# Kernel tuning notes

Measured on AMD Instinct MI355X. Metric: run time of the kernel, lower is better.

Reference implementation:

```python
import jax, jax.numpy as jnp
import numpy as np

D_MODEL = 1024
NUM_HEADS = 16
DEPTH = D_MODEL // NUM_HEADS
B, S = 2, 2048


def setup_inputs() -> dict:
    key = jax.random.key(0)
    ks = jax.random.split(key, 12)
    s = 1.0 / np.sqrt(D_MODEL)
    return {
        "query": jax.random.normal(ks[0], (B, S, D_MODEL), jnp.float32),
        "key": jax.random.normal(ks[1], (B, S, D_MODEL), jnp.float32),
        "value": jax.random.normal(ks[2], (B, S, D_MODEL), jnp.float32),
        "mask": jax.random.randint(ks[3], (B, S), 0, 2, jnp.int32),
        "Wq": jax.random.normal(ks[4], (D_MODEL, D_MODEL), jnp.float32) * s,
        "bq": jnp.zeros((D_MODEL,), jnp.float32),
        "Wk": jax.random.normal(ks[5], (D_MODEL, D_MODEL), jnp.float32) * s,
        "bk": jnp.zeros((D_MODEL,), jnp.float32),
        "Wv": jax.random.normal(ks[6], (D_MODEL, D_MODEL), jnp.float32) * s,
        "bv": jnp.zeros((D_MODEL,), jnp.float32),
        "Wo": jax.random.normal(ks[7], (D_MODEL, D_MODEL), jnp.float32) * s,
        "bo": jnp.zeros((D_MODEL,), jnp.float32),
    }


def _split_heads(x):
    # [B, S, D] -> [B, H, S, depth]
    b, s, _ = x.shape
    return x.reshape(b, s, NUM_HEADS, DEPTH).transpose(0, 2, 1, 3)


def reference(query, key, value, mask, Wq, bq, Wk, bk, Wv, bv, Wo, bo):
    q = _split_heads(query @ Wq.T + bq)
    k = _split_heads(key @ Wk.T + bk)
    v = _split_heads(value @ Wv.T + bv)
    scale = 1.0 / jnp.sqrt(jnp.float32(DEPTH))
    # [B, H, Sq, Sk]
    logits = jnp.einsum("bhqd,bhkd->bhqk", q, k) * scale
    logits = logits + mask.astype(logits.dtype)[:, None, None, :] * (-1e9)
    attn = jax.nn.softmax(logits, axis=-1)
    out = jnp.einsum("bhqk,bhkd->bhqd", attn, v)
    out = out.transpose(0, 2, 1, 3).reshape(query.shape[0], -1, D_MODEL)
    return out @ Wo.T + bo
```

## Files before the change

### kernel.cpp

```cpp
#include <hip/hip_runtime.h>

typedef _Float16 half8 __attribute__((ext_vector_type(8)));
typedef float floatx4 __attribute__((ext_vector_type(4)));

#define D_MODEL 1024
#define NHEAD   16
#define DH      64
#define BATCH   2
#define SEQ     2048
#define M_TOT   4096

#define GLD_LDS16(g, l)                                                          \
  __builtin_amdgcn_global_load_lds(                                              \
      (const __attribute__((address_space(1))) void*)(g),                        \
      (__attribute__((address_space(3))) void*)(l), 16, 0, 0)

__global__ __launch_bounds__(256) void cvt_all(const float* __restrict__ q,
                                               const float* __restrict__ k,
                                               const float* __restrict__ v,
                                               const float* __restrict__ wq,
                                               const float* __restrict__ wk,
                                               const float* __restrict__ wv,
                                               const float* __restrict__ wo,
                                               _Float16* __restrict__ Xall,
                                               _Float16* __restrict__ Wall) {
  int bid = blockIdx.x;
  const float* src;
  _Float16* dst;
  if (bid < 6144) {
    int tsr = bid >> 11;
    src = (tsr == 0) ? q : (tsr == 1) ? k : v;
    dst = Xall + (size_t)tsr * 4194304;
    bid &= 2047;
  } else {
    int w = (bid - 6144) >> 9;
    src = (w == 0) ? wq : (w == 1) ? wk : (w == 2) ? wv : wo;
    dst = Wall + (size_t)w * 1048576;
    bid = (bid - 6144) & 511;
  }
  int off = bid * 2048 + threadIdx.x * 8;
  float4 a = *(const float4*)(src + off);
  float4 b = *(const float4*)(src + off + 4);
  half8 h;
  h[0] = (_Float16)a.x; h[1] = (_Float16)a.y; h[2] = (_Float16)a.z; h[3] = (_Float16)a.w;
  h[4] = (_Float16)b.x; h[5] = (_Float16)b.y; h[6] = (_Float16)b.z; h[7] = (_Float16)b.w;
  *(half8*)(dst + off) = h;
}

__global__ __launch_bounds__(256) void gemm_qkv(const _Float16* __restrict__ Xall,
                                                const _Float16* __restrict__ Wall,
                                                const float* __restrict__ bq,
                                                const float* __restrict__ bk,
                                                const float* __restrict__ bv,
                                                _Float16* __restrict__ Obase) {
  __shared__ alignas(16) char smem[17408];
  _Float16 (*As)[32]  = (_Float16(*)[32])smem;
  _Float16 (*Bs)[32]  = (_Float16(*)[32])(smem + 8192);
  _Float16 (*Ts)[136] = (_Float16(*)[136])smem;

  const int z = blockIdx.z;
  const _Float16* X = Xall + (size_t)z * 4194304;
  const _Float16* W = Wall + (size_t)z * 1048576;
  const float* bias = (z == 0) ? bq : (z == 1) ? bk : bv;
  _Float16* out = Obase + (size_t)z * 4194304;

  const int t = threadIdx.x, lane = t & 63, wave = t >> 6;
  const int wr = wave >> 1, wc = wave & 1;
  const int m0 = blockIdx.y * 128, n0 = blockIdx.x * 128;
  const int fr = lane & 15, fc = (lane >> 4) * 8, rg = (lane >> 4) * 4;

  floatx4 acc[4][4];
  for (int i = 0; i < 4; i++)
    for (int j = 0; j < 4; j++) acc[i][j] = (floatx4){0.f, 0.f, 0.f, 0.f};

  const int srow = lane >> 2, scol = (lane & 3) * 8;
  const _Float16* gA0 = X + (size_t)(m0 + wave * 32 + srow) * 1024 + scol;
  const _Float16* gA1 = gA0 + 16 * 1024;
  const _Float16* gB0 = W + (size_t)(n0 + wave * 32 + srow) * 1024 + scol;
  const _Float16* gB1 = gB0 + 16 * 1024;
  _Float16* lA0 = &As[wave * 32][0];
  _Float16* lA1 = &As[wave * 32 + 16][0];
  _Float16* lB0 = &Bs[wave * 32][0];
  _Float16* lB1 = &Bs[wave * 32 + 16][0];

  for (int k0 = 0; k0 < 1024; k0 += 32) {
    GLD_LDS16(gA0 + k0, lA0);
    GLD_LDS16(gA1 + k0, lA1);
    GLD_LDS16(gB0 + k0, lB0);
    GLD_LDS16(gB1 + k0, lB1);
    __syncthreads();

    half8 af[4], bw[4];
    for (int i = 0; i < 4; i++) {
      af[i] = *(const half8*)&As[wr * 64 + i * 16 + fr][fc];
      bw[i] = *(const half8*)&Bs[wc * 64 + i * 16 + fr][fc];
    }
    for (int i = 0; i < 4; i++)
      for (int j = 0; j < 4; j++)
        acc[i][j] = __builtin_amdgcn_mfma_f32_16x16x32_f16(af[i], bw[j], acc[i][j], 0, 0, 0);
    __syncthreads();
  }

  if (z != 2) {
    for (int i = 0; i < 4; i++)
      for (int j = 0; j < 4; j++) {
        int n = n0 + wc * 64 + j * 16 + fr;
        float bv2 = bias[n];
        int hh = n >> 6, d = n & 63;
        for (int r = 0; r < 4; r++) {
          int m = m0 + wr * 64 + i * 16 + rg + r;
          int bb = m >> 11, s = m & 2047;
          out[(((size_t)(bb * NHEAD + hh)) * SEQ + s) * DH + d] =
              (_Float16)(acc[i][j][r] + bv2);
        }
      }
  } else {
    const int bb = m0 >> 11, s0 = m0 & 2047;
    for (int p = 0; p < 2; p++) {
      __syncthreads();
      if (wc == p) {
        for (int j = 0; j < 4; j++) {
          float bv2 = bias[n0 + p * 64 + j * 16 + fr];
          for (int i = 0; i < 4; i++)
            for (int r = 0; r < 4; r++)
              Ts[j * 16 + fr][wr * 64 + i * 16 + rg + r] =
                  (_Float16)(acc[i][j][r] + bv2);
        }
      }
      __syncthreads();
      int dd = t >> 2, c4 = (t & 3) * 32;
      int hh = (n0 >> 6) + p;
      _Float16* dst = out + (((size_t)(bb * NHEAD + hh)) * DH + dd) * SEQ + s0;
      for (int u = 0; u < 4; u++)
        *(half8*)(dst + c4 + u * 8) = *(const half8*)&Ts[dd][c4 + u * 8];
    }
  }
}

__global__ __launch_bounds__(256) void gemm_wo(const _Float16* __restrict__ ctx,
                                               const _Float16* __restrict__ W,
                                               const float* __restrict__ bias,
                                               float* __restrict__ out) {
  __shared__ alignas(16) _Float16 As[128][32];
  __shared__ alignas(16) _Float16 Bs[64][32];

  const int t = threadIdx.x, lane = t & 63, wave = t >> 6;
  const int m0 = blockIdx.y * 128, n0 = blockIdx.x * 64;
  const int fr = lane & 15, fc = (lane >> 4) * 8, rg = (lane >> 4) * 4;

  floatx4 acc[2][4];
  for (int i = 0; i < 2; i++)
    for (int j = 0; j < 4; j++) acc[i][j] = (floatx4){0.f, 0.f, 0.f, 0.f};

  const int srow = lane >> 2, scol = (lane & 3) * 8;
  const _Float16* gA0 = ctx + (size_t)(m0 + wave * 32 + srow) * 1024 + scol;
  const _Float16* gA1 = gA0 + 16 * 1024;
  const _Float16* gB0 = W + (size_t)(n0 + wave * 16 + srow) * 1024 + scol;
  _Float16* lA0 = &As[wave * 32][0];
  _Float16* lA1 = &As[wave * 32 + 16][0];
  _Float16* lB0 = &Bs[wave * 16][0];

  for (int k0 = 0; k0 < 1024; k0 += 32) {
    GLD_LDS16(gA0 + k0, lA0);
    GLD_LDS16(gA1 + k0, lA1);
    GLD_LDS16(gB0 + k0, lB0);
    __syncthreads();

    half8 af[2], bw[4];
    for (int i = 0; i < 2; i++)
      af[i] = *(const half8*)&As[wave * 32 + i * 16 + fr][fc];
    for (int j = 0; j < 4; j++)
      bw[j] = *(const half8*)&Bs[j * 16 + fr][fc];
    for (int i = 0; i < 2; i++)
      for (int j = 0; j < 4; j++)
        acc[i][j] = __builtin_amdgcn_mfma_f32_16x16x32_f16(af[i], bw[j], acc[i][j], 0, 0, 0);
    __syncthreads();
  }

  for (int i = 0; i < 2; i++)
    for (int j = 0; j < 4; j++) {
      int n = n0 + j * 16 + fr;
      float bv2 = bias[n];
      for (int r = 0; r < 4; r++) {
        int m = m0 + wave * 32 + i * 16 + rg + r;
        out[(size_t)m * D_MODEL + n] = acc[i][j][r] + bv2;
      }
    }
}

__global__ __launch_bounds__(256) void attn_kernel(const _Float16* __restrict__ Qp,
                                                   const _Float16* __restrict__ Kp,
                                                   const _Float16* __restrict__ VT,
                                                   const int* __restrict__ mask,
                                                   _Float16* __restrict__ ctx) {
  __shared__ alignas(16) char lds[17408 + 34816 + 512];
  _Float16 (*Vt)[136] = (_Float16(*)[136])lds;
  _Float16 (*Ks)[72]  = (_Float16(*)[72])(lds + 17408);
  _Float16 (*Ps)[136] = (_Float16(*)[136])(lds + 17408);
  float* Ms = (float*)(lds + 17408 + 34816);

  const int b = blockIdx.z, h = blockIdx.y, q0 = blockIdx.x * 128;
  const int t = threadIdx.x, lane = t & 63, wave = t >> 6;
  const int fr = lane & 15, fc = (lane >> 4) * 8, rg = (lane >> 4) * 4;

  const _Float16* Kg  = Kp + (size_t)(b * NHEAD + h) * SEQ * DH;
  const _Float16* VTg = VT + (size_t)(b * NHEAD + h) * DH * SEQ;

  half8 qf[2][2];
  {
    const _Float16* Qgw = Qp + ((size_t)(b * NHEAD + h) * SEQ + q0 + wave * 32) * DH;
    for (int mi = 0; mi < 2; mi++)
      for (int kk = 0; kk < 2; kk++)
        qf[mi][kk] = *(const half8*)(Qgw + (mi * 16 + fr) * DH + kk * 32 + fc);
  }

  float mrow[2][4], lrow[2][4];
  floatx4 oacc[2][4];
  for (int mi = 0; mi < 2; mi++)
    for (int r = 0; r < 4; r++) { mrow[mi][r] = -3.0e38f; lrow[mi][r] = 0.f; }
  for (int mi = 0; mi < 2; mi++)
    for (int dj = 0; dj < 4; dj++) oacc[mi][dj] = (floatx4){0.f, 0.f, 0.f, 0.f};

  for (int kt = 0; kt < SEQ / 128; kt++) {
    const int k0 = kt * 128;
    {
      int r = t >> 1, c0 = (t & 1) * 32;
      const half8* gk = (const half8*)(Kg + (k0 + r) * 64 + c0);
      for (int u = 0; u < 4; u++)
        *(half8*)&Ks[r][c0 + u * 8] = gk[u];
      int dd = t >> 2, c4 = (t & 3) * 32;
      const _Float16* gv = VTg + (size_t)dd * SEQ + k0 + c4;
      for (int u = 0; u < 4; u++)
        *(half8*)&Vt[dd][c4 + u * 8] = *(const half8*)(gv + u * 8);
      if (t < 128) Ms[t] = (float)mask[b * SEQ + k0 + t] * -1.0e9f;
    }
    __syncthreads();

    floatx4 sa[2][8];
    for (int mi = 0; mi < 2; mi++)
      for (int nj = 0; nj < 8; nj++) sa[mi][nj] = (floatx4){0.f, 0.f, 0.f, 0.f};
    for (int nj = 0; nj < 8; nj++)
      for (int kk = 0; kk < 2; kk++) {
        half8 kf = *(const half8*)&Ks[nj * 16 + fr][kk * 32 + fc];
        sa[0][nj] = __builtin_amdgcn_mfma_f32_16x16x32_f16(qf[0][kk], kf, sa[0][nj], 0, 0, 0);
        sa[1][nj] = __builtin_amdgcn_mfma_f32_16x16x32_f16(qf[1][kk], kf, sa[1][nj], 0, 0, 0);
      }
    __syncthreads();

    for (int nj = 0; nj < 8; nj++) {
      float mk = Ms[nj * 16 + fr];
      for (int mi = 0; mi < 2; mi++)
        for (int r = 0; r < 4; r++)
          sa[mi][nj][r] = sa[mi][nj][r] * 0.125f + mk;
    }

    for (int mi = 0; mi < 2; mi++) {
      for (int r = 0; r < 4; r++) {
        float tm = sa[mi][0][r];
        for (int nj = 1; nj < 8; nj++) tm = fmaxf(tm, sa[mi][nj][r]);
        for (int off = 1; off < 16; off <<= 1) tm = fmaxf(tm, __shfl_xor(tm, off));
        float mnew = fmaxf(mrow[mi][r], tm);
        float alpha = __expf(mrow[mi][r] - mnew);
        mrow[mi][r] = mnew;
        float rs = 0.f;
        for (int nj = 0; nj < 8; nj++) {
          float p = __expf(sa[mi][nj][r] - mnew);
          sa[mi][nj][r] = p;
          rs += p;
        }
        for (int off = 1; off < 16; off <<= 1) rs += __shfl_xor(rs, off);
        lrow[mi][r] = lrow[mi][r] * alpha + rs;
        for (int dj = 0; dj < 4; dj++) oacc[mi][dj][r] *= alpha;
      }
    }

    for (int mi = 0; mi < 2; mi++)
      for (int nj = 0; nj < 8; nj++)
        for (int r = 0; r < 4; r++)
          Ps[wave * 32 + mi * 16 + rg + r][nj * 16 + fr] = (_Float16)sa[mi][nj][r];
    __syncthreads();

    for (int kk = 0; kk < 4; kk++) {
      half8 pf[2], vf[4];
      for (int mi = 0; mi < 2; mi++)
        pf[mi] = *(const half8*)&Ps[wave * 32 + mi * 16 + fr][kk * 32 + fc];
      for (int dj = 0; dj < 4; dj++)
        vf[dj] = *(const half8*)&Vt[dj * 16 + fr][kk * 32 + fc];
      for (int mi = 0; mi < 2; mi++)
        for (int dj = 0; dj < 4; dj++)
          oacc[mi][dj] = __builtin_amdgcn_mfma_f32_16x16x32_f16(pf[mi], vf[dj], oacc[mi][dj], 0, 0, 0);
    }
    __syncthreads();
  }

  for (int mi = 0; mi < 2; mi++)
    for (int r = 0; r < 4; r++) {
      float inv = 1.0f / lrow[mi][r];
      int qrow = q0 + wave * 32 + mi * 16 + rg + r;
      _Float16* o = ctx + ((size_t)b * SEQ + qrow) * D_MODEL + h * DH;
      for (int dj = 0; dj < 4; dj++)
        o[dj * 16 + fr] = (_Float16)(oacc[mi][dj][r] * inv);
    }
}

extern "C" void kernel_launch(void* const* d_in, const int* in_sizes, int n_in,
                              void* d_out, int out_size, void* d_ws, size_t ws_size,
                              hipStream_t stream) {
  const float* query = (const float*)d_in[0];
  const float* key   = (const float*)d_in[1];
  const float* value = (const float*)d_in[2];
  const int*   mask  = (const int*)d_in[3];
  const float* Wq = (const float*)d_in[4];
  const float* bq = (const float*)d_in[5];
  const float* Wk = (const float*)d_in[6];
  const float* bk = (const float*)d_in[7];
  const float* Wv = (const float*)d_in[8];
  const float* bv = (const float*)d_in[9];
  const float* Wo = (const float*)d_in[10];
  const float* bo = (const float*)d_in[11];

  char* ws = (char*)d_ws;
  _Float16* Xall = (_Float16*)(ws);
  _Float16* Wall = (_Float16*)(ws + (size_t)24 * 1024 * 1024);
  _Float16* Qp   = (_Float16*)(ws + (size_t)32 * 1024 * 1024);
  _Float16* ctx  = (_Float16*)(ws + (size_t)56 * 1024 * 1024);

  _Float16* Kp = Qp + (size_t)4194304;
  _Float16* VT = Qp + (size_t)8388608;

  cvt_all<<<8192, 256, 0, stream>>>(query, key, value, Wq, Wk, Wv, Wo, Xall, Wall);

  gemm_qkv<<<dim3(8, 32, 3), 256, 0, stream>>>(Xall, Wall, bq, bk, bv, Qp);

  attn_kernel<<<dim3(SEQ / 128, NHEAD, BATCH), 256, 0, stream>>>(Qp, Kp, VT, mask, ctx);

  gemm_wo<<<dim3(16, 32), 256, 0, stream>>>(ctx, Wall + (size_t)3 * 1048576, bo, (float*)d_out);
}
```

Before: 285.3 us.

## Compute transposed scores so P stays in registers, skipping LDS round-trip

The attention kernel now computes S^T = K·Q^T with MFMA, so each lane holds a column of scores for one query row. That lets the softmax P feed the PV MFMA (16x16x16) directly from registers, with no Ps write to LDS and two fewer barriers per key tile. Softmax uses exp2 with the scale and mask folded into a log2(e) factor, and row reductions need only two cross-lane shuffles. In exchange, the PV MFMA uses the smaller 16x16x16 shape, and P is converted to fp16 with round-toward-zero packing.

```diff
diff --git a/kernel.cpp b/kernel.cpp
--- a/kernel.cpp
+++ b/kernel.cpp
@@ -1,6 +1,8 @@
 #include <hip/hip_runtime.h>
 
 typedef _Float16 half8 __attribute__((ext_vector_type(8)));
+typedef _Float16 half4 __attribute__((ext_vector_type(4)));
+typedef __fp16  fp16x2 __attribute__((ext_vector_type(2)));
 typedef float floatx4 __attribute__((ext_vector_type(4)));
 
 #define D_MODEL 1024
@@ -10,10 +12,20 @@
 #define SEQ     2048
 #define M_TOT   4096
 
+#define SCALE_L2E 0.18033688011112042f
+#define MASK_L2E  (-1.4426950408889634e9f)
+
 #define GLD_LDS16(g, l)                                                          \
   __builtin_amdgcn_global_load_lds(                                              \
       (const __attribute__((address_space(1))) void*)(g),                        \
       (__attribute__((address_space(3))) void*)(l), 16, 0, 0)
+
+__device__ inline half4 pk4(floatx4 v) {
+  union { fp16x2 h2[2]; half4 h4; } u;
+  u.h2[0] = __builtin_amdgcn_cvt_pkrtz(v[0], v[1]);
+  u.h2[1] = __builtin_amdgcn_cvt_pkrtz(v[2], v[3]);
+  return u.h4;
+}
 
 __global__ __launch_bounds__(256) void cvt_all(const float* __restrict__ q,
                                                const float* __restrict__ k,
@@ -193,15 +205,13 @@
                                                    const _Float16* __restrict__ VT,
                                                    const int* __restrict__ mask,
                                                    _Float16* __restrict__ ctx) {
-  __shared__ alignas(16) char lds[17408 + 34816 + 512];
-  _Float16 (*Vt)[136] = (_Float16(*)[136])lds;
-  _Float16 (*Ks)[72]  = (_Float16(*)[72])(lds + 17408);
-  _Float16 (*Ps)[136] = (_Float16(*)[136])(lds + 17408);
-  float* Ms = (float*)(lds + 17408 + 34816);
+  __shared__ alignas(16) _Float16 Ks[128][72];
+  __shared__ alignas(16) _Float16 Vt[64][136];
+  __shared__ float Msf[128];
 
   const int b = blockIdx.z, h = blockIdx.y, q0 = blockIdx.x * 128;
   const int t = threadIdx.x, lane = t & 63, wave = t >> 6;
-  const int fr = lane & 15, fc = (lane >> 4) * 8, rg = (lane >> 4) * 4;
+  const int fr = lane & 15, quad = lane >> 4, fc = quad * 8;
 
   const _Float16* Kg  = Kp + (size_t)(b * NHEAD + h) * SEQ * DH;
   const _Float16* VTg = VT + (size_t)(b * NHEAD + h) * DH * SEQ;
@@ -214,12 +224,10 @@
         qf[mi][kk] = *(const half8*)(Qgw + (mi * 16 + fr) * DH + kk * 32 + fc);
   }
 
-  float mrow[2][4], lrow[2][4];
-  floatx4 oacc[2][4];
-  for (int mi = 0; mi < 2; mi++)
-    for (int r = 0; r < 4; r++) { mrow[mi][r] = -3.0e38f; lrow[mi][r] = 0.f; }
-  for (int mi = 0; mi < 2; mi++)
-    for (int dj = 0; dj < 4; dj++) oacc[mi][dj] = (floatx4){0.f, 0.f, 0.f, 0.f};
+  float mrow[2] = {-3.0e38f, -3.0e38f}, lrow[2] = {0.f, 0.f};
+  floatx4 oaccT[4][2];
+  for (int dj = 0; dj < 4; dj++)
+    for (int mi = 0; mi < 2; mi++) oaccT[dj][mi] = (floatx4){0.f, 0.f, 0.f, 0.f};
 
   for (int kt = 0; kt < SEQ / 128; kt++) {
     const int k0 = kt * 128;
@@ -232,75 +240,86 @@
       const _Float16* gv = VTg + (size_t)dd * SEQ + k0 + c4;
       for (int u = 0; u < 4; u++)
         *(half8*)&Vt[dd][c4 + u * 8] = *(const half8*)(gv + u * 8);
-      if (t < 128) Ms[t] = (float)mask[b * SEQ + k0 + t] * -1.0e9f;
-    }
-    __syncthreads();
-
-    floatx4 sa[2][8];
-    for (int mi = 0; mi < 2; mi++)
-      for (int nj = 0; nj < 8; nj++) sa[mi][nj] = (floatx4){0.f, 0.f, 0.f, 0.f};
-    for (int nj = 0; nj < 8; nj++)
-      for (int kk = 0; kk < 2; kk++) {
-        half8 kf = *(const half8*)&Ks[nj * 16 + fr][kk * 32 + fc];
-        sa[0][nj] = __builtin_amdgcn_mfma_f32_16x16x32_f16(qf[0][kk], kf, sa[0][nj], 0, 0, 0);
-        sa[1][nj] = __builtin_amdgcn_mfma_f32_16x16x32_f16(qf[1][kk], kf, sa[1][nj], 0, 0, 0);
-      }
-    __syncthreads();
-
-    for (int nj = 0; nj < 8; nj++) {
-      float mk = Ms[nj * 16 + fr];
-      for (int mi = 0; mi < 2; mi++)
+      if (t < 128) Msf[t] = (float)mask[b * SEQ + k0 + t] * MASK_L2E;
+    }
+    __syncthreads();
+
+    floatx4 saT[8][2];
+#pragma unroll
+    for (int t8 = 0; t8 < 8; t8++) {
+      saT[t8][0] = (floatx4){0.f, 0.f, 0.f, 0.f};
+      saT[t8][1] = (floatx4){0.f, 0.f, 0.f, 0.f};
+      half8 kf0 = *(const half8*)&Ks[t8 * 16 + fr][fc];
+      half8 kf1 = *(const half8*)&Ks[t8 * 16 + fr][32 + fc];
+      saT[t8][0] = __builtin_amdgcn_mfma_f32_16x16x32_f16(kf0, qf[0][0], saT[t8][0], 0, 0, 0);
+      saT[t8][1] = __builtin_amdgcn_mfma_f32_16x16x32_f16(kf0, qf[1][0], saT[t8][1], 0, 0, 0);
+      saT[t8][0] = __builtin_amdgcn_mfma_f32_16x16x32_f16(kf1, qf[0][1], saT[t8][0], 0, 0, 0);
+      saT[t8][1] = __builtin_amdgcn_mfma_f32_16x16x32_f16(kf1, qf[1][1], saT[t8][1], 0, 0, 0);
+    }
+
+    floatx4 mk[8];
+#pragma unroll
+    for (int t8 = 0; t8 < 8; t8++)
+      mk[t8] = *(const floatx4*)&Msf[t8 * 16 + quad * 4];
+
+    float alpha[2];
+#pragma unroll
+    for (int mi = 0; mi < 2; mi++) {
+#pragma unroll
+      for (int t8 = 0; t8 < 8; t8++)
         for (int r = 0; r < 4; r++)
-          sa[mi][nj][r] = sa[mi][nj][r] * 0.125f + mk;
-    }
-
-    for (int mi = 0; mi < 2; mi++) {
-      for (int r = 0; r < 4; r++) {
-        float tm = sa[mi][0][r];
-        for (int nj = 1; nj < 8; nj++) tm = fmaxf(tm, sa[mi][nj][r]);
-        for (int off = 1; off < 16; off <<= 1) tm = fmaxf(tm, __shfl_xor(tm, off));
-        float mnew = fmaxf(mrow[mi][r], tm);
-        float alpha = __expf(mrow[mi][r] - mnew);
-        mrow[mi][r] = mnew;
-        float rs = 0.f;
-        for (int nj = 0; nj < 8; nj++) {
-          float p = __expf(sa[mi][nj][r] - mnew);
-          sa[mi][nj][r] = p;
+          saT[t8][mi][r] = saT[t8][mi][r] * SCALE_L2E + mk[t8][r];
+      float tm = saT[0][mi][0];
+#pragma unroll
+      for (int t8 = 0; t8 < 8; t8++)
+        for (int r = 0; r < 4; r++) tm = fmaxf(tm, saT[t8][mi][r]);
+      tm = fmaxf(tm, __shfl_xor(tm, 16));
+      tm = fmaxf(tm, __shfl_xor(tm, 32));
+      float mnew = fmaxf(mrow[mi], tm);
+      alpha[mi] = exp2f(mrow[mi] - mnew);
+      mrow[mi] = mnew;
+      float rs = 0.f;
+#pragma unroll
+      for (int t8 = 0; t8 < 8; t8++)
+        for (int r = 0; r < 4; r++) {
+          float p = exp2f(saT[t8][mi][r] - mnew);
+          saT[t8][mi][r] = p;
           rs += p;
         }
-        for (int off = 1; off < 16; off <<= 1) rs += __shfl_xor(rs, off);
-        lrow[mi][r] = lrow[mi][r] * alpha + rs;
-        for (int dj = 0; dj < 4; dj++) oacc[mi][dj][r] *= alpha;
+      rs += __shfl_xor(rs, 16);
+      rs += __shfl_xor(rs, 32);
+      lrow[mi] = lrow[mi] * alpha[mi] + rs;
+#pragma unroll
+      for (int dj = 0; dj < 4; dj++)
+        for (int r = 0; r < 4; r++) oaccT[dj][mi][r] *= alpha[mi];
+    }
+
+#pragma unroll
+    for (int t8 = 0; t8 < 8; t8++) {
+      half4 pb0 = pk4(saT[t8][0]);
+      half4 pb1 = pk4(saT[t8][1]);
+#pragma unroll
+      for (int dj = 0; dj < 4; dj++) {
+        half4 va = *(const half4*)&Vt[dj * 16 + fr][t8 * 16 + quad * 4];
+        oaccT[dj][0] = __builtin_amdgcn_mfma_f32_16x16x16f16(va, pb0, oaccT[dj][0], 0, 0, 0);
+        oaccT[dj][1] = __builtin_amdgcn_mfma_f32_16x16x16f16(va, pb1, oaccT[dj][1], 0, 0, 0);
       }
     }
-
-    for (int mi = 0; mi < 2; mi++)
-      for (int nj = 0; nj < 8; nj++)
-        for (int r = 0; r < 4; r++)
-          Ps[wave * 32 + mi * 16 + rg + r][nj * 16 + fr] = (_Float16)sa[mi][nj][r];
-    __syncthreads();
-
-    for (int kk = 0; kk < 4; kk++) {
-      half8 pf[2], vf[4];
-      for (int mi = 0; mi < 2; mi++)
-        pf[mi] = *(const half8*)&Ps[wave * 32 + mi * 16 + fr][kk * 32 + fc];
-      for (int dj = 0; dj < 4; dj++)
-        vf[dj] = *(const half8*)&Vt[dj * 16 + fr][kk * 32 + fc];
-      for (int mi = 0; mi < 2; mi++)
-        for (int dj = 0; dj < 4; dj++)
-          oacc[mi][dj] = __builtin_amdgcn_mfma_f32_16x16x32_f16(pf[mi], vf[dj], oacc[mi][dj], 0, 0, 0);
-    }
-    __syncthreads();
-  }
-
-  for (int mi = 0; mi < 2; mi++)
-    for (int r = 0; r < 4; r++) {
-      float inv = 1.0f / lrow[mi][r];
-      int qrow = q0 + wave * 32 + mi * 16 + rg + r;
-      _Float16* o = ctx + ((size_t)b * SEQ + qrow) * D_MODEL + h * DH;
-      for (int dj = 0; dj < 4; dj++)
-        o[dj * 16 + fr] = (_Float16)(oacc[mi][dj][r] * inv);
-    }
+    __syncthreads();
+  }
+
+#pragma unroll
+  for (int mi = 0; mi < 2; mi++) {
+    float inv = 1.0f / lrow[mi];
+    int qrow = q0 + wave * 32 + mi * 16 + fr;
+    _Float16* o = ctx + ((size_t)b * SEQ + qrow) * D_MODEL + h * DH;
+#pragma unroll
+    for (int dj = 0; dj < 4; dj++) {
+      half4 st;
+      for (int r = 0; r < 4; r++) st[r] = (_Float16)(oaccT[dj][mi][r] * inv);
+      *(half4*)(o + dj * 16 + quad * 4) = st;
+    }
+  }
 }
 
 extern "C" void kernel_launch(void* const* d_in, const int* in_sizes, int n_in,
```

New measurement: 276.4 us. 3.1% less time.
